# Kernel tuning notes

Measured on AMD Instinct MI355X. Metric: run time of the kernel, lower is better.

The kernel has to match this reference:

```python
import jax, jax.numpy as jnp
import numpy as np

B, T, C, NH = 8, 1024, 768, 12
HD = C // NH


def setup_inputs() -> dict:
    key = jax.random.key(0)
    k1, k2, k3, k4, k5 = jax.random.split(key, 5)
    s = 0.02
    return {
        "x": jax.random.normal(k1, (B, T, C), dtype=jnp.float32),
        "w_attn": jax.random.normal(k2, (C, 3 * C), dtype=jnp.float32) * s,
        "b_attn": jax.random.normal(k3, (3 * C,), dtype=jnp.float32) * s,
        "w_proj": jax.random.normal(k4, (C, C), dtype=jnp.float32) * s,
        "b_proj": jax.random.normal(k5, (C,), dtype=jnp.float32) * s,
    }


def reference(x, w_attn, b_attn, w_proj, b_proj):
    Bv, Tv, Cv = x.shape
    # fused QKV projection
    qkv = jnp.einsum('btc,cd->btd', x, w_attn) + b_attn  # [B,T,3C]
    q, k, v = jnp.split(qkv, 3, axis=-1)
    # [B, NH, T, HD]
    q = q.reshape(Bv, Tv, NH, HD).transpose(0, 2, 1, 3)
    k = k.reshape(Bv, Tv, NH, HD).transpose(0, 2, 1, 3)
    v = v.reshape(Bv, Tv, NH, HD).transpose(0, 2, 1, 3)
    scale = 1.0 / np.sqrt(HD).astype(np.float32)
    att = jnp.einsum('bhqd,bhkd->bhqk', q, k) * scale  # [B,NH,T,T]
    causal = jnp.tril(jnp.ones((Tv, Tv), dtype=bool))
    att = jnp.where(causal, att, -jnp.inf)
    att = jax.nn.softmax(att, axis=-1)
    y = jnp.einsum('bhqk,bhkd->bhqd', att, v)  # [B,NH,T,HD]
    y = y.transpose(0, 2, 1, 3).reshape(Bv, Tv, Cv)
    return jnp.einsum('btc,cd->btd', y, w_proj) + b_proj
```

## Files before the change

kernel.cpp:

```cpp
#include <hip/hip_runtime.h>

constexpr int kB  = 8;
constexpr int kT  = 1024;
constexpr int kC  = 768;
constexpr int kNH = 12;
constexpr int kHD = 64;
constexpr int kM  = kB * kT;
constexpr int k3C = 3 * kC;
constexpr int kQK = 2 * kC;

using bf16x8 = __attribute__((ext_vector_type(8))) __bf16;
using f32x4  = __attribute__((ext_vector_type(4))) float;

__device__ __forceinline__ unsigned short f2bf(float f) {
    union { float f; unsigned int u; } v; v.f = f;
    unsigned int r = v.u + 0x7fffu + ((v.u >> 16) & 1u);
    return (unsigned short)(r >> 16);
}

__device__ __forceinline__ void async16(const void* g, void* l) {
    __builtin_amdgcn_global_load_lds(
        (__attribute__((address_space(1))) void*)g,
        (__attribute__((address_space(3))) void*)l, 16, 0, 0);
}

template<int IMM> __device__ __forceinline__ void wait_vm() {
    __builtin_amdgcn_s_waitcnt(IMM);
}
__device__ __forceinline__ void wait_vm0() { __builtin_amdgcn_s_waitcnt(0x0F70); }


__global__ __launch_bounds__(256) void cvt_bf16_kernel(
    const float* __restrict__ in, unsigned short* __restrict__ out)
{
    const int i = blockIdx.x * 256 + threadIdx.x;
    const float4 v = ((const float4*)in)[i];
    ushort4 o;
    o.x = f2bf(v.x); o.y = f2bf(v.y); o.z = f2bf(v.z); o.w = f2bf(v.w);
    ((ushort4*)out)[i] = o;
}

__global__ __launch_bounds__(256) void transpose_cvt_kernel(
    const float* __restrict__ W, unsigned short* __restrict__ Wt, int K, int N)
{
    __shared__ float tile[32][33];
    const int tx = threadIdx.x & 31, ty = threadIdx.x >> 5;
    const int n0 = blockIdx.x * 32, k0 = blockIdx.y * 32;
    #pragma unroll
    for (int i = 0; i < 4; ++i)
        tile[ty + i * 8][tx] = W[(size_t)(k0 + ty + i * 8) * N + n0 + tx];
    __syncthreads();
    #pragma unroll
    for (int i = 0; i < 4; ++i)
        Wt[(size_t)(n0 + ty + i * 8) * K + k0 + tx] = f2bf(tile[tx][ty + i * 8]);
}

template<int NSUB, int MODE, int K>
__global__ __launch_bounds__(256) void gemm_mfma_kernel(
    const unsigned short* __restrict__ A,
    const unsigned short* __restrict__ Bt,
    const float* __restrict__ bias,
    void* __restrict__ outv,
    unsigned short* __restrict__ vt,
    int N)
{
    constexpr int NW = NSUB / 2;
    constexpr int BB = (NSUB / 4 > 0) ? NSUB / 4 : 1;
    constexpr int P  = 2 + BB;
    constexpr int WAIT_P = 0x0F70 | P;
    constexpr int NITER = K / 32;

    alignas(16) __shared__ unsigned short As[3][8 * 512];
    alignas(16) __shared__ unsigned short Bs[3][NSUB * 512];

    const int tid  = threadIdx.x;
    const int w    = tid >> 6;
    const int lane = tid & 63;
    const int wr = w >> 1, wc = w & 1;
    const int m0 = blockIdx.x * 128;
    const int n0 = blockIdx.y * (NSUB * 16);

    const int fr = lane & 15;
    const int fk = (lane >> 4) * 8;

    auto stage = [&](int bufi, int kt) {
        #pragma unroll
        for (int t = 0; t < 2; ++t) {
            const int fa = w * 2 + t;
            const unsigned short* ga =
                A + (size_t)(m0 + fa * 16 + fr) * K + kt + fk;
            async16(ga, &As[bufi][fa * 512]);
        }
        #pragma unroll
        for (int t = 0; t < BB; ++t) {
            const int fb = w * BB + t;
            const unsigned short* gb =
                Bt + (size_t)(n0 + fb * 16 + fr) * K + kt + fk;
            async16(gb, &Bs[bufi][fb * 512]);
        }
    };

    f32x4 acc[4][NW];
    #pragma unroll
    for (int i = 0; i < 4; ++i)
        #pragma unroll
        for (int j = 0; j < NW; ++j) {
            f32x4 z = {0.f, 0.f, 0.f, 0.f};
            acc[i][j] = z;
        }

    stage(0, 0);
    stage(1, 32);
    for (int it3 = 0; it3 < NITER; it3 += 3) {
        #pragma unroll
        for (int u = 0; u < 3; ++u) {
            const int it = it3 + u;
            if (it + 1 < NITER) wait_vm<WAIT_P>();
            else                wait_vm<0x0F70>();
            __builtin_amdgcn_s_barrier();
            if (it + 2 < NITER) stage((u + 2) % 3, (it + 2) * 32);

            bf16x8 a[4], b[NW];
            #pragma unroll
            for (int i = 0; i < 4; ++i)
                a[i] = *(const bf16x8*)&As[u][(wr * 4 + i) * 512 + lane * 8];
            #pragma unroll
            for (int j = 0; j < NW; ++j)
                b[j] = *(const bf16x8*)&Bs[u][(wc * NW + j) * 512 + lane * 8];
            #pragma unroll
            for (int i = 0; i < 4; ++i)
                #pragma unroll
                for (int j = 0; j < NW; ++j)
                    acc[i][j] = __builtin_amdgcn_mfma_f32_16x16x32_bf16(
                        a[i], b[j], acc[i][j], 0, 0, 0);
        }
    }

    const int quad  = lane >> 4;
    const int col16 = lane & 15;
    float biasv[NW];
    #pragma unroll
    for (int j = 0; j < NW; ++j)
        biasv[j] = bias[n0 + wc * (NW * 16) + j * 16 + col16];

    if (MODE == 1 && n0 >= kQK) {
        const int bidx = m0 >> 10;
        #pragma unroll
        for (int i = 0; i < 4; ++i) {
            const int t = (m0 + wr * 64 + i * 16 + quad * 4) & 1023;
            #pragma unroll
            for (int j = 0; j < NW; ++j) {
                const int hv = n0 + wc * (NW * 16) + j * 16 + col16 - kQK;
                const int h = hv >> 6, d = hv & 63;
                ushort4 o;
                o.x = f2bf(acc[i][j][0] + biasv[j]);
                o.y = f2bf(acc[i][j][1] + biasv[j]);
                o.z = f2bf(acc[i][j][2] + biasv[j]);
                o.w = f2bf(acc[i][j][3] + biasv[j]);
                *(ushort4*)&vt[((size_t)(bidx * kNH + h) * kHD + d) * kT + t] = o;
            }
        }
    } else {
        #pragma unroll
        for (int i = 0; i < 4; ++i) {
            #pragma unroll
            for (int r = 0; r < 4; ++r) {
                const int row = m0 + wr * 64 + i * 16 + quad * 4 + r;
                #pragma unroll
                for (int j = 0; j < NW; ++j) {
                    const int col = n0 + wc * (NW * 16) + j * 16 + col16;
                    const float v = acc[i][j][r] + biasv[j];
                    if (MODE == 1)
                        ((unsigned short*)outv)[(size_t)row * kQK + col] = f2bf(v);
                    else
                        ((float*)outv)[(size_t)row * N + col] = v;
                }
            }
        }
    }
}

__global__ __launch_bounds__(256) void attn_mfma_kernel(
    const unsigned short* __restrict__ qkv2,
    const unsigned short* __restrict__ VT,
    unsigned short* __restrict__ y)
{
    alignas(16) __shared__ unsigned short Kf[2][8 * 512];
    alignas(16) __shared__ unsigned short Vf[2][8 * 512];
    alignas(16) __shared__ unsigned short Pf[8 * 512];

    const int tid  = threadIdx.x;
    const int w    = tid >> 6;
    const int lane = tid & 63;
    const int quad = lane >> 4, l15 = lane & 15;
    const int bh  = blockIdx.x >> 3;
    const int b   = bh / kNH, h = bh % kNH;
    const int pid = blockIdx.x & 7;

    auto stage = [&](int bufi, int kbase) {
        const unsigned short* gk = qkv2 +
            (size_t)(b * kT + kbase + w * 16 + l15) * kQK + kC + h * kHD + quad * 8;
        async16(gk,      &Kf[bufi][(w * 2 + 0) * 512]);
        async16(gk + 32, &Kf[bufi][(w * 2 + 1) * 512]);
        const unsigned short* gv = VT +
            ((size_t)bh * kHD + w * 16 + l15) * kT + kbase + quad * 8;
        async16(gv,      &Vf[bufi][(w * 2 + 0) * 512]);
        async16(gv + 32, &Vf[bufi][(w * 2 + 1) * 512]);
    };

    #pragma unroll 1
    for (int phase = 0; phase < 2; ++phase) {
        const int t0 = (phase == 0 ? (15 - pid) : pid) * 64;
        const int nchunks = t0 / 64 + 1;

        __syncthreads();
        stage(0, 0);
        {
            const unsigned short* g0 = qkv2 +
                (size_t)(b * kT + t0 + w * 16 + l15) * kQK + h * kHD + quad * 8;
            async16(g0,      &Pf[(w * 2 + 0) * 512]);
            async16(g0 + 32, &Pf[(w * 2 + 1) * 512]);
        }
        wait_vm0();
        const bf16x8 aq0 = *(const bf16x8*)&Pf[(w * 2 + 0) * 512 + lane * 8];
        const bf16x8 aq1 = *(const bf16x8*)&Pf[(w * 2 + 1) * 512 + lane * 8];

        float m_run[4], l_run[4];
        f32x4 acc_o[4];
        #pragma unroll
        for (int r = 0; r < 4; ++r) { m_run[r] = -INFINITY; l_run[r] = 0.f; }
        #pragma unroll
        for (int n = 0; n < 4; ++n) {
            f32x4 z = {0.f, 0.f, 0.f, 0.f};
            acc_o[n] = z;
        }

        for (int c = 0; c < nchunks; ++c) {
            const int kbase = c * 64;
            const int buf = c & 1;
            wait_vm0();
            __syncthreads();
            if (c + 1 < nchunks) stage(1 - buf, kbase + 64);

            f32x4 acc_s[4];
            #pragma unroll
            for (int k = 0; k < 4; ++k) {
                f32x4 z = {0.f, 0.f, 0.f, 0.f};
                acc_s[k] = z;
            }
            #pragma unroll
            for (int ksub = 0; ksub < 4; ++ksub) {
                const bf16x8 bk0 =
                    *(const bf16x8*)&Kf[buf][(ksub * 2 + 0) * 512 + lane * 8];
                const bf16x8 bk1 =
                    *(const bf16x8*)&Kf[buf][(ksub * 2 + 1) * 512 + lane * 8];
                acc_s[ksub] = __builtin_amdgcn_mfma_f32_16x16x32_bf16(
                    aq0, bk0, acc_s[ksub], 0, 0, 0);
                acc_s[ksub] = __builtin_amdgcn_mfma_f32_16x16x32_bf16(
                    aq1, bk1, acc_s[ksub], 0, 0, 0);
            }

            float sv[4][4];
            #pragma unroll
            for (int ksub = 0; ksub < 4; ++ksub)
                #pragma unroll
                for (int r = 0; r < 4; ++r)
                    sv[ksub][r] = acc_s[ksub][r] * 0.125f;
            if (kbase == t0) {
                const int qrow = t0 + w * 16 + quad * 4;
                #pragma unroll
                for (int ksub = 0; ksub < 4; ++ksub) {
                    const int key = kbase + ksub * 16 + l15;
                    #pragma unroll
                    for (int r = 0; r < 4; ++r)
                        if (key > qrow + r) sv[ksub][r] = -INFINITY;
                }
            }

            float alpha[4];
            #pragma unroll
            for (int r = 0; r < 4; ++r) {
                float mx = fmaxf(fmaxf(sv[0][r], sv[1][r]),
                                 fmaxf(sv[2][r], sv[3][r]));
                mx = fmaxf(mx, __shfl_xor(mx, 1));
                mx = fmaxf(mx, __shfl_xor(mx, 2));
                mx = fmaxf(mx, __shfl_xor(mx, 4));
                mx = fmaxf(mx, __shfl_xor(mx, 8));
                const float m_new = fmaxf(m_run[r], mx);
                alpha[r] = __expf(m_run[r] - m_new);
                float ps = 0.f;
                #pragma unroll
                for (int ksub = 0; ksub < 4; ++ksub) {
                    sv[ksub][r] = __expf(sv[ksub][r] - m_new);
                    ps += sv[ksub][r];
                }
                ps += __shfl_xor(ps, 1);
                ps += __shfl_xor(ps, 2);
                ps += __shfl_xor(ps, 4);
                ps += __shfl_xor(ps, 8);
                l_run[r] = l_run[r] * alpha[r] + ps;
                m_run[r] = m_new;
            }

            #pragma unroll
            for (int ksub = 0; ksub < 4; ++ksub) {
                const int key = ksub * 16 + l15;
                #pragma unroll
                for (int r = 0; r < 4; ++r) {
                    const int lp = quad * 4 + r + ((key & 31) >> 3) * 16;
                    Pf[(w * 2 + (key >> 5)) * 512 + lp * 8 + (key & 7)] =
                        f2bf(sv[ksub][r]);
                }
            }

            #pragma unroll
            for (int n = 0; n < 4; ++n)
                #pragma unroll
                for (int r = 0; r < 4; ++r)
                    acc_o[n][r] *= alpha[r];
            const bf16x8 ap0 = *(const bf16x8*)&Pf[(w * 2 + 0) * 512 + lane * 8];
            const bf16x8 ap1 = *(const bf16x8*)&Pf[(w * 2 + 1) * 512 + lane * 8];
            #pragma unroll
            for (int nsub = 0; nsub < 4; ++nsub) {
                const bf16x8 bv0 =
                    *(const bf16x8*)&Vf[buf][(nsub * 2 + 0) * 512 + lane * 8];
                const bf16x8 bv1 =
                    *(const bf16x8*)&Vf[buf][(nsub * 2 + 1) * 512 + lane * 8];
                acc_o[nsub] = __builtin_amdgcn_mfma_f32_16x16x32_bf16(
                    ap0, bv0, acc_o[nsub], 0, 0, 0);
                acc_o[nsub] = __builtin_amdgcn_mfma_f32_16x16x32_bf16(
                    ap1, bv1, acc_o[nsub], 0, 0, 0);
            }
        }

        float inv[4];
        #pragma unroll
        for (int r = 0; r < 4; ++r) inv[r] = 1.0f / l_run[r];
        #pragma unroll
        for (int nsub = 0; nsub < 4; ++nsub)
            #pragma unroll
            for (int r = 0; r < 4; ++r)
                y[(size_t)(b * kT + t0 + w * 16 + quad * 4 + r) * kC +
                  h * kHD + nsub * 16 + l15] = f2bf(acc_o[nsub][r] * inv[r]);
    }
}

extern "C" void kernel_launch(void* const* d_in, const int* in_sizes, int n_in,
                              void* d_out, int out_size, void* d_ws, size_t ws_size,
                              hipStream_t stream) {
    const float* x      = (const float*)d_in[0];
    const float* w_attn = (const float*)d_in[1];
    const float* b_attn = (const float*)d_in[2];
    const float* w_proj = (const float*)d_in[3];
    const float* b_proj = (const float*)d_in[4];
    float* out = (float*)d_out;

    unsigned short* xb     = (unsigned short*)d_ws;
    unsigned short* wattnT = xb     + (size_t)kM * kC;
    unsigned short* wprojT = wattnT + (size_t)k3C * kC;
    unsigned short* qkv2   = wprojT + (size_t)kC * kC;
    unsigned short* VT     = qkv2   + (size_t)kM * kQK;
    unsigned short* yb     = VT     + (size_t)kNH * kB * kHD * kT;

    cvt_bf16_kernel<<<(kM * kC) / (4 * 256), 256, 0, stream>>>(x, xb);
    transpose_cvt_kernel<<<dim3(k3C / 32, kC / 32), 256, 0, stream>>>(
        w_attn, wattnT, kC, k3C);
    transpose_cvt_kernel<<<dim3(kC / 32, kC / 32), 256, 0, stream>>>(
        w_proj, wprojT, kC, kC);

    gemm_mfma_kernel<8, 1, kC><<<dim3(kM / 128, k3C / 128), 256, 0, stream>>>(
        xb, wattnT, b_attn, qkv2, VT, k3C);

    attn_mfma_kernel<<<kB * kNH * 8, 256, 0, stream>>>(qkv2, VT, yb);

    gemm_mfma_kernel<4, 0, kC><<<dim3(kM / 128, kC / 64), 256, 0, stream>>>(
        yb, wprojT, b_proj, out, nullptr, kC);
}
```

Baseline: 235.3 us.

## Share K/V chunk loads between paired query tiles in one pass

Each block now processes its two causal query tiles (the late tile 15-pid and the early tile pid) in a single loop over key chunks, so K and V chunks are staged once and reused by both tiles instead of being reloaded in a second phase. The row-sum shuffle reduction is also moved out of the per-chunk loop and done once before normalization, since the per-lane partial sums combine linearly. In exchange the block keeps two sets of accumulators and Q fragments live, which raises register pressure. The two tiles' work within a chunk is serialized through the shared P buffer.

```diff
diff --git a/kernel.cpp b/kernel.cpp
--- a/kernel.cpp
+++ b/kernel.cpp
@@ -196,6 +196,9 @@
     const int bh  = blockIdx.x >> 3;
     const int b   = bh / kNH, h = bh % kNH;
     const int pid = blockIdx.x & 7;
+    const int t0A = (15 - pid) * 64;
+    const int t0B = pid * 64;
+    const int nch = 16 - pid;
 
     auto stage = [&](int bufi, int kbase) {
         const unsigned short* gk = qkv2 +
@@ -208,141 +211,160 @@
         async16(gv + 32, &Vf[bufi][(w * 2 + 1) * 512]);
     };
 
-    #pragma unroll 1
-    for (int phase = 0; phase < 2; ++phase) {
-        const int t0 = (phase == 0 ? (15 - pid) : pid) * 64;
-        const int nchunks = t0 / 64 + 1;
-
-        __syncthreads();
-        stage(0, 0);
-        {
-            const unsigned short* g0 = qkv2 +
-                (size_t)(b * kT + t0 + w * 16 + l15) * kQK + h * kHD + quad * 8;
-            async16(g0,      &Pf[(w * 2 + 0) * 512]);
-            async16(g0 + 32, &Pf[(w * 2 + 1) * 512]);
-        }
+    stage(0, 0);
+    bf16x8 aqA0, aqA1, aqB0, aqB1;
+    {
+        const unsigned short* gA = qkv2 +
+            (size_t)(b * kT + t0A + w * 16 + l15) * kQK + h * kHD + quad * 8;
+        async16(gA,      &Pf[(w * 2 + 0) * 512]);
+        async16(gA + 32, &Pf[(w * 2 + 1) * 512]);
         wait_vm0();
-        const bf16x8 aq0 = *(const bf16x8*)&Pf[(w * 2 + 0) * 512 + lane * 8];
-        const bf16x8 aq1 = *(const bf16x8*)&Pf[(w * 2 + 1) * 512 + lane * 8];
-
-        float m_run[4], l_run[4];
-        f32x4 acc_o[4];
-        #pragma unroll
-        for (int r = 0; r < 4; ++r) { m_run[r] = -INFINITY; l_run[r] = 0.f; }
-        #pragma unroll
-        for (int n = 0; n < 4; ++n) {
+        aqA0 = *(const bf16x8*)&Pf[(w * 2 + 0) * 512 + lane * 8];
+        aqA1 = *(const bf16x8*)&Pf[(w * 2 + 1) * 512 + lane * 8];
+        const unsigned short* gB = qkv2 +
+            (size_t)(b * kT + t0B + w * 16 + l15) * kQK + h * kHD + quad * 8;
+        async16(gB,      &Pf[(w * 2 + 0) * 512]);
+        async16(gB + 32, &Pf[(w * 2 + 1) * 512]);
+        wait_vm0();
+        aqB0 = *(const bf16x8*)&Pf[(w * 2 + 0) * 512 + lane * 8];
+        aqB1 = *(const bf16x8*)&Pf[(w * 2 + 1) * 512 + lane * 8];
+    }
+
+    float mA[4], lA[4], mB[4], lB[4];
+    f32x4 oA[4], oB[4];
+    #pragma unroll
+    for (int r = 0; r < 4; ++r) {
+        mA[r] = -INFINITY; lA[r] = 0.f;
+        mB[r] = -INFINITY; lB[r] = 0.f;
+    }
+    #pragma unroll
+    for (int n = 0; n < 4; ++n) {
+        f32x4 z = {0.f, 0.f, 0.f, 0.f};
+        oA[n] = z; oB[n] = z;
+    }
+
+    auto chunk_compute = [&](const bf16x8& q0, const bf16x8& q1,
+                             float* m_run, float* l_run, f32x4* acc_o,
+                             int t0, int kbase, int buf, bool diag) {
+        f32x4 acc_s[4];
+        #pragma unroll
+        for (int k = 0; k < 4; ++k) {
             f32x4 z = {0.f, 0.f, 0.f, 0.f};
-            acc_o[n] = z;
-        }
-
-        for (int c = 0; c < nchunks; ++c) {
-            const int kbase = c * 64;
-            const int buf = c & 1;
-            wait_vm0();
-            __syncthreads();
-            if (c + 1 < nchunks) stage(1 - buf, kbase + 64);
-
-            f32x4 acc_s[4];
-            #pragma unroll
-            for (int k = 0; k < 4; ++k) {
-                f32x4 z = {0.f, 0.f, 0.f, 0.f};
-                acc_s[k] = z;
-            }
+            acc_s[k] = z;
+        }
+        #pragma unroll
+        for (int ksub = 0; ksub < 4; ++ksub) {
+            const bf16x8 bk0 =
+                *(const bf16x8*)&Kf[buf][(ksub * 2 + 0) * 512 + lane * 8];
+            const bf16x8 bk1 =
+                *(const bf16x8*)&Kf[buf][(ksub * 2 + 1) * 512 + lane * 8];
+            acc_s[ksub] = __builtin_amdgcn_mfma_f32_16x16x32_bf16(
+                q0, bk0, acc_s[ksub], 0, 0, 0);
+            acc_s[ksub] = __builtin_amdgcn_mfma_f32_16x16x32_bf16(
+                q1, bk1, acc_s[ksub], 0, 0, 0);
+        }
+
+        float sv[4][4];
+        #pragma unroll
+        for (int ksub = 0; ksub < 4; ++ksub)
+            #pragma unroll
+            for (int r = 0; r < 4; ++r)
+                sv[ksub][r] = acc_s[ksub][r] * 0.125f;
+        if (diag) {
+            const int qrow = t0 + w * 16 + quad * 4;
             #pragma unroll
             for (int ksub = 0; ksub < 4; ++ksub) {
-                const bf16x8 bk0 =
-                    *(const bf16x8*)&Kf[buf][(ksub * 2 + 0) * 512 + lane * 8];
-                const bf16x8 bk1 =
-                    *(const bf16x8*)&Kf[buf][(ksub * 2 + 1) * 512 + lane * 8];
-                acc_s[ksub] = __builtin_amdgcn_mfma_f32_16x16x32_bf16(
-                    aq0, bk0, acc_s[ksub], 0, 0, 0);
-                acc_s[ksub] = __builtin_amdgcn_mfma_f32_16x16x32_bf16(
-                    aq1, bk1, acc_s[ksub], 0, 0, 0);
-            }
-
-            float sv[4][4];
-            #pragma unroll
-            for (int ksub = 0; ksub < 4; ++ksub)
+                const int key = kbase + ksub * 16 + l15;
                 #pragma unroll
                 for (int r = 0; r < 4; ++r)
-                    sv[ksub][r] = acc_s[ksub][r] * 0.125f;
-            if (kbase == t0) {
-                const int qrow = t0 + w * 16 + quad * 4;
-                #pragma unroll
-                for (int ksub = 0; ksub < 4; ++ksub) {
-                    const int key = kbase + ksub * 16 + l15;
-                    #pragma unroll
-                    for (int r = 0; r < 4; ++r)
-                        if (key > qrow + r) sv[ksub][r] = -INFINITY;
-                }
+                    if (key > qrow + r) sv[ksub][r] = -INFINITY;
             }
-
-            float alpha[4];
+        }
+
+        float alpha[4];
+        #pragma unroll
+        for (int r = 0; r < 4; ++r) {
+            float mx = fmaxf(fmaxf(sv[0][r], sv[1][r]),
+                             fmaxf(sv[2][r], sv[3][r]));
+            mx = fmaxf(mx, __shfl_xor(mx, 1));
+            mx = fmaxf(mx, __shfl_xor(mx, 2));
+            mx = fmaxf(mx, __shfl_xor(mx, 4));
+            mx = fmaxf(mx, __shfl_xor(mx, 8));
+            const float m_new = fmaxf(m_run[r], mx);
+            alpha[r] = __expf(m_run[r] - m_new);
+            float ps = 0.f;
+            #pragma unroll
+            for (int ksub = 0; ksub < 4; ++ksub) {
+                sv[ksub][r] = __expf(sv[ksub][r] - m_new);
+                ps += sv[ksub][r];
+            }
+            l_run[r] = l_run[r] * alpha[r] + ps;
+            m_run[r] = m_new;
+        }
+
+        #pragma unroll
+        for (int ksub = 0; ksub < 4; ++ksub) {
+            const int key = ksub * 16 + l15;
             #pragma unroll
             for (int r = 0; r < 4; ++r) {
-                float mx = fmaxf(fmaxf(sv[0][r], sv[1][r]),
-                                 fmaxf(sv[2][r], sv[3][r]));
-                mx = fmaxf(mx, __shfl_xor(mx, 1));
-                mx = fmaxf(mx, __shfl_xor(mx, 2));
-                mx = fmaxf(mx, __shfl_xor(mx, 4));
-                mx = fmaxf(mx, __shfl_xor(mx, 8));
-                const float m_new = fmaxf(m_run[r], mx);
-                alpha[r] = __expf(m_run[r] - m_new);
-                float ps = 0.f;
-                #pragma unroll
-                for (int ksub = 0; ksub < 4; ++ksub) {
-                    sv[ksub][r] = __expf(sv[ksub][r] - m_new);
-                    ps += sv[ksub][r];
-                }
-                ps += __shfl_xor(ps, 1);
-                ps += __shfl_xor(ps, 2);
-                ps += __shfl_xor(ps, 4);
-                ps += __shfl_xor(ps, 8);
-                l_run[r] = l_run[r] * alpha[r] + ps;
-                m_run[r] = m_new;
+                const int lp = quad * 4 + r + ((key & 31) >> 3) * 16;
+                Pf[(w * 2 + (key >> 5)) * 512 + lp * 8 + (key & 7)] =
+                    f2bf(sv[ksub][r]);
             }
-
-            #pragma unroll
-            for (int ksub = 0; ksub < 4; ++ksub) {
-                const int key = ksub * 16 + l15;
-                #pragma unroll
-                for (int r = 0; r < 4; ++r) {
-                    const int lp = quad * 4 + r + ((key & 31) >> 3) * 16;
-                    Pf[(w * 2 + (key >> 5)) * 512 + lp * 8 + (key & 7)] =
-                        f2bf(sv[ksub][r]);
-                }
-            }
-
-            #pragma unroll
-            for (int n = 0; n < 4; ++n)
-                #pragma unroll
-                for (int r = 0; r < 4; ++r)
-                    acc_o[n][r] *= alpha[r];
-            const bf16x8 ap0 = *(const bf16x8*)&Pf[(w * 2 + 0) * 512 + lane * 8];
-            const bf16x8 ap1 = *(const bf16x8*)&Pf[(w * 2 + 1) * 512 + lane * 8];
-            #pragma unroll
-            for (int nsub = 0; nsub < 4; ++nsub) {
-                const bf16x8 bv0 =
-                    *(const bf16x8*)&Vf[buf][(nsub * 2 + 0) * 512 + lane * 8];
-                const bf16x8 bv1 =
-                    *(const bf16x8*)&Vf[buf][(nsub * 2 + 1) * 512 + lane * 8];
-                acc_o[nsub] = __builtin_amdgcn_mfma_f32_16x16x32_bf16(
-                    ap0, bv0, acc_o[nsub], 0, 0, 0);
-                acc_o[nsub] = __builtin_amdgcn_mfma_f32_16x16x32_bf16(
-                    ap1, bv1, acc_o[nsub], 0, 0, 0);
-            }
-        }
-
+        }
+
+        #pragma unroll
+        for (int n = 0; n < 4; ++n)
+            #pragma unroll
+            for (int r = 0; r < 4; ++r)
+                acc_o[n][r] *= alpha[r];
+        const bf16x8 ap0 = *(const bf16x8*)&Pf[(w * 2 + 0) * 512 + lane * 8];
+        const bf16x8 ap1 = *(const bf16x8*)&Pf[(w * 2 + 1) * 512 + lane * 8];
+        #pragma unroll
+        for (int nsub = 0; nsub < 4; ++nsub) {
+            const bf16x8 bv0 =
+                *(const bf16x8*)&Vf[buf][(nsub * 2 + 0) * 512 + lane * 8];
+            const bf16x8 bv1 =
+                *(const bf16x8*)&Vf[buf][(nsub * 2 + 1) * 512 + lane * 8];
+            acc_o[nsub] = __builtin_amdgcn_mfma_f32_16x16x32_bf16(
+                ap0, bv0, acc_o[nsub], 0, 0, 0);
+            acc_o[nsub] = __builtin_amdgcn_mfma_f32_16x16x32_bf16(
+                ap1, bv1, acc_o[nsub], 0, 0, 0);
+        }
+    };
+
+    for (int c = 0; c < nch; ++c) {
+        const int kbase = c * 64;
+        const int buf = c & 1;
+        wait_vm0();
+        __syncthreads();
+        if (c + 1 < nch) stage(1 - buf, kbase + 64);
+
+        chunk_compute(aqA0, aqA1, mA, lA, oA, t0A, kbase, buf, kbase == t0A);
+        if (c <= pid)
+            chunk_compute(aqB0, aqB1, mB, lB, oB, t0B, kbase, buf, kbase == t0B);
+    }
+
+    auto write_tile = [&](float* l_run, f32x4* acc_o, int t0) {
         float inv[4];
         #pragma unroll
-        for (int r = 0; r < 4; ++r) inv[r] = 1.0f / l_run[r];
+        for (int r = 0; r < 4; ++r) {
+            float s = l_run[r];
+            s += __shfl_xor(s, 1);
+            s += __shfl_xor(s, 2);
+            s += __shfl_xor(s, 4);
+            s += __shfl_xor(s, 8);
+            inv[r] = 1.0f / s;
+        }
         #pragma unroll
         for (int nsub = 0; nsub < 4; ++nsub)
             #pragma unroll
             for (int r = 0; r < 4; ++r)
                 y[(size_t)(b * kT + t0 + w * 16 + quad * 4 + r) * kC +
                   h * kHD + nsub * 16 + l15] = f2bf(acc_o[nsub][r] * inv[r]);
-    }
+    };
+    write_tile(lA, oA, t0A);
+    write_tile(lB, oB, t0B);
 }
 
 extern "C" void kernel_launch(void* const* d_in, const int* in_sizes, int n_in,
```

Result: slower. 252.0 us (+7.1%).
